# Kernel tuning notes

Measured on AMD Instinct MI355X. Metric: run time of the kernel, lower is better.

The kernel has to match this reference:

```python
import jax, jax.numpy as jnp
import numpy as np

B, S, F, H = 16, 2048, 1024, 16
D = F // H
EPS = 1e-5


def setup_inputs() -> dict:
    key = jax.random.key(0)
    ks = jax.random.split(key, 10)
    scale = 1.0 / np.sqrt(F)
    return {
        "x": jax.random.normal(ks[0], (B, S, F), jnp.float32),
        "Wq": jax.random.normal(ks[1], (F, F), jnp.float32) * scale,
        "bq": jnp.zeros((F,), jnp.float32),
        "Wk": jax.random.normal(ks[2], (F, F), jnp.float32) * scale,
        "bk": jnp.zeros((F,), jnp.float32),
        "Wv": jax.random.normal(ks[3], (F, F), jnp.float32) * scale,
        "bv": jnp.zeros((F,), jnp.float32),
        "Wo": jax.random.normal(ks[4], (F, F), jnp.float32) * scale,
        "bo": jnp.zeros((F,), jnp.float32),
        "gamma": jnp.ones((F,), jnp.float32),
        "beta": jnp.zeros((F,), jnp.float32),
    }


def reference(x, Wq, bq, Wk, bk, Wv, bv, Wo, bo, gamma, beta):
    # x: (B, S, F). Dropout is identity in eval mode.
    b, s, f = x.shape
    q = (x @ Wq + bq).reshape(b, s, H, D)
    k = (x @ Wk + bk).reshape(b, s, H, D)
    v = (x @ Wv + bv).reshape(b, s, H, D)
    # Faithful to source: the einsum (applied to permuted tensors) contracts
    # across HEADS at each sequence position -> scores (B, S, H, H).
    energy = jnp.einsum('bshd,bsgd->bshg', q, k) / (D ** 0.5)
    attn = jax.nn.softmax(energy, axis=-1)  # softmax over key-head axis
    out = jnp.einsum('bshg,bsgd->bshd', attn, v).reshape(b, s, f)
    out = out @ Wo + bo
    # LayerNorm over last dim (eps=1e-5, affine)
    mu = jnp.mean(out, axis=-1, keepdims=True)
    var = jnp.mean((out - mu) ** 2, axis=-1, keepdims=True)
    return (out - mu) * jax.lax.rsqrt(var + EPS) * gamma + beta
```

## Files before the change

### kernel.cpp

```cpp
#include <hip/hip_runtime.h>
#include <hip/hip_bf16.h>
#include <stdint.h>

#define MM   32768
#define FFD  1024
#define NQKV 3072

typedef __bf16 bf16x8 __attribute__((ext_vector_type(8)));
typedef float  f32x4  __attribute__((ext_vector_type(4)));

__device__ __forceinline__ unsigned short f2bf_bits(float f){
  __hip_bfloat16 h = __float2bfloat16(f);
  unsigned short u;
  __builtin_memcpy(&u, &h, 2);
  return u;
}

__device__ __forceinline__ void gld16(const void* g, void* l){
  const unsigned int* gu = (const unsigned int*)g;
  unsigned int* lu = (unsigned int*)l;
  __builtin_amdgcn_global_load_lds(
      (const __attribute__((address_space(1))) unsigned int*)gu,
      (__attribute__((address_space(3))) unsigned int*)lu,
      16, 0, 0);
}

__global__ __launch_bounds__(256) void k_convert_bf16(const float* __restrict__ in,
                                                      unsigned short* __restrict__ out,
                                                      int n4){
  int i = blockIdx.x * 256 + threadIdx.x;
  if (i >= n4) return;
  float4 v = ((const float4*)in)[i];
  ushort4 r;
  r.x = f2bf_bits(v.x); r.y = f2bf_bits(v.y);
  r.z = f2bf_bits(v.z); r.w = f2bf_bits(v.w);
  ((ushort4*)out)[i] = r;
}

__global__ __launch_bounds__(256) void k_transpose_bf16(const float* __restrict__ in,
                                                        unsigned short* __restrict__ out,
                                                        int rows, int cols){
  __shared__ float tile[32][33];
  int bc = blockIdx.x * 32, br = blockIdx.y * 32;
  int tx = threadIdx.x, ty = threadIdx.y;
  #pragma unroll
  for (int j = 0; j < 32; j += 8)
    tile[ty + j][tx] = in[(size_t)(br + ty + j) * cols + bc + tx];
  __syncthreads();
  #pragma unroll
  for (int j = 0; j < 32; j += 8)
    out[(size_t)(bc + ty + j) * rows + br + tx] = f2bf_bits(tile[tx][ty + j]);
}

template <bool BF16OUT>
__global__ __launch_bounds__(256) void k_gemm_bt(
    const unsigned short* __restrict__ A,
    const unsigned short* __restrict__ Bt,
    const float* __restrict__ b0, const float* __restrict__ b1, const float* __restrict__ b2,
    void* __restrict__ Cout, int M, int N, int K)
{
  __shared__ unsigned short As[128 * 64];
  __shared__ unsigned short Bs[128 * 64];

  const int tid  = threadIdx.x;
  const int lane = tid & 63;
  const int wave = tid >> 6;
  const int wr = wave >> 1, wc = wave & 1;
  const int quad = lane >> 4, lrow = lane & 15;

  const long rowBase = (long)blockIdx.y * 128;
  const long colBase = (long)blockIdx.x * 128;

  f32x4 acc[4][4];
  #pragma unroll
  for (int i = 0; i < 4; i++)
    #pragma unroll
    for (int j = 0; j < 4; j++)
      acc[i][j] = (f32x4){0.f, 0.f, 0.f, 0.f};

  const unsigned short* ga = A  + (rowBase + (tid >> 2)) * (long)K + (tid & 3) * 8;
  const unsigned short* gb = Bt + (colBase + (tid >> 2)) * (long)K + (tid & 3) * 8;
  unsigned short* la = As + tid * 8;
  unsigned short* lb = Bs + tid * 8;
  const long rstep = 64L * K;

  const int nk = K >> 6;
  for (int kt = 0; kt < nk; kt++){
    __syncthreads();
    gld16(ga,               la);
    gld16(ga + rstep,       la + 2048);
    gld16(ga + 32,          la + 4096);
    gld16(ga + 32 + rstep,  la + 6144);
    gld16(gb,               lb);
    gld16(gb + rstep,       lb + 2048);
    gld16(gb + 32,          lb + 4096);
    gld16(gb + 32 + rstep,  lb + 6144);
    __syncthreads();

    #pragma unroll
    for (int kk = 0; kk < 2; kk++){
      const unsigned short* Ah = As + kk * 4096;
      const unsigned short* Bh = Bs + kk * 4096;
      bf16x8 af[4], bfr[4];
      #pragma unroll
      for (int i = 0; i < 4; i++)
        af[i]  = *(const bf16x8*)(Ah + (wr * 64 + i * 16 + lrow) * 32 + quad * 8);
      #pragma unroll
      for (int j = 0; j < 4; j++)
        bfr[j] = *(const bf16x8*)(Bh + (wc * 64 + j * 16 + lrow) * 32 + quad * 8);

      #pragma unroll
      for (int i = 0; i < 4; i++)
        #pragma unroll
        for (int j = 0; j < 4; j++)
          acc[i][j] = __builtin_amdgcn_mfma_f32_16x16x32_bf16(af[i], bfr[j], acc[i][j], 0, 0, 0);
    }

    ga += 64; gb += 64;
  }

  #pragma unroll
  for (int j = 0; j < 4; j++){
    long col = colBase + wc * 64 + j * 16 + lrow;
    const float* bp = (col < 1024) ? b0 : ((col < 2048) ? b1 : b2);
    float bias = bp[col & 1023];
    #pragma unroll
    for (int i = 0; i < 4; i++){
      long row0 = rowBase + wr * 64 + i * 16 + quad * 4;
      #pragma unroll
      for (int r = 0; r < 4; r++){
        float v = acc[i][j][r] + bias;
        if constexpr (BF16OUT)
          ((unsigned short*)Cout)[(row0 + r) * (long)N + col] = f2bf_bits(v);
        else
          ((float*)Cout)[(row0 + r) * (long)N + col] = v;
      }
    }
  }
}

__global__ __launch_bounds__(256) void k_attention(const unsigned short* __restrict__ qkv,
                                                   unsigned short* __restrict__ aout){
  constexpr int QOFF = 0;
  constexpr int KOFF = 1152;
  constexpr int VOFF = 2304;
  constexpr int POFF = 4864;
  constexpr int PER  = 5504;
  __shared__ unsigned short smem[4 * PER];

  const int lane = threadIdx.x & 63;
  const int wave = threadIdx.x >> 6;
  const int pos  = blockIdx.x * 4 + wave;
  const int quad = lane >> 4, lidx = lane & 15;

  unsigned short* base = smem + wave * PER;
  unsigned short* Qb = base + QOFF;
  unsigned short* Kb = base + KOFF;
  unsigned short* Vt = base + VOFF;
  unsigned short* Pb = base + POFF;

  {
    uint4 z = {0u, 0u, 0u, 0u};
    *(uint4*)(Vt + lane * 40 + 16) = z;
    *(uint4*)(Vt + lane * 40 + 24) = z;
    *(uint2*)(Pb + (lane >> 2) * 40 + 16 + (lane & 3) * 4) = make_uint2(0u, 0u);
  }

  const unsigned short* src = qkv + (size_t)pos * 3072;
  #pragma unroll
  for (int i = 0; i < 6; i++){
    int c = i * 64 + lane;
    uint4 u = *(const uint4*)(src + c * 8);
    if (i < 4){
      unsigned short* mb = (c < 128) ? Qb : Kb;
      int cc = c & 127;
      *(uint4*)(mb + (cc >> 3) * 72 + (cc & 7) * 8) = u;
    } else {
      int cv = c - 256;
      int g = cv >> 3, d0 = (cv & 7) * 8;
      const unsigned short* us = (const unsigned short*)&u;
      #pragma unroll
      for (int t = 0; t < 8; t++) Vt[(d0 + t) * 40 + g] = us[t];
    }
  }
  __syncthreads();

  f32x4 s = (f32x4){0.f, 0.f, 0.f, 0.f};
  #pragma unroll
  for (int kk = 0; kk < 2; kk++){
    bf16x8 a = *(const bf16x8*)(Qb + lidx * 72 + kk * 32 + quad * 8);
    bf16x8 b = *(const bf16x8*)(Kb + lidx * 72 + kk * 32 + quad * 8);
    s = __builtin_amdgcn_mfma_f32_16x16x32_bf16(a, b, s, 0, 0, 0);
  }

  #pragma unroll
  for (int r = 0; r < 4; r++){
    float v = s[r] * 0.125f;
    float m = v;
    m = fmaxf(m, __shfl_xor(m, 1));
    m = fmaxf(m, __shfl_xor(m, 2));
    m = fmaxf(m, __shfl_xor(m, 4));
    m = fmaxf(m, __shfl_xor(m, 8));
    float e = __expf(v - m);
    float sum = e;
    sum += __shfl_xor(sum, 1);
    sum += __shfl_xor(sum, 2);
    sum += __shfl_xor(sum, 4);
    sum += __shfl_xor(sum, 8);
    float p = e / sum;
    Pb[(quad * 4 + r) * 40 + lidx] = f2bf_bits(p);
  }
  __syncthreads();

  f32x4 o[4];
  #pragma unroll
  for (int n4 = 0; n4 < 4; n4++){
    bf16x8 a = *(const bf16x8*)(Pb + lidx * 40 + quad * 8);
    bf16x8 b = *(const bf16x8*)(Vt + (n4 * 16 + lidx) * 40 + quad * 8);
    o[n4] = __builtin_amdgcn_mfma_f32_16x16x32_bf16(a, b, (f32x4){0.f,0.f,0.f,0.f}, 0, 0, 0);
  }

  #pragma unroll
  for (int n4 = 0; n4 < 4; n4++)
    #pragma unroll
    for (int r = 0; r < 4; r++)
      Qb[(quad * 4 + r) * 72 + n4 * 16 + lidx] = f2bf_bits(o[n4][r]);
  __syncthreads();

  unsigned short* dst = aout + (size_t)pos * 1024;
  #pragma unroll
  for (int t = 0; t < 2; t++){
    int j = lane * 2 + t;
    int h = j >> 3, dc = j & 7;
    uint4 u = *(const uint4*)(Qb + h * 72 + dc * 8);
    *(uint4*)(dst + j * 8) = u;
  }
}

__global__ __launch_bounds__(256) void k_ln(float* __restrict__ out,
                                            const float* __restrict__ gamma,
                                            const float* __restrict__ beta){
  __shared__ float red[8];
  int tid = threadIdx.x;
  float4* rowp = (float4*)(out + (size_t)blockIdx.x * 1024);
  float4 v = rowp[tid];
  float s  = v.x + v.y + v.z + v.w;
  float ss = v.x * v.x + v.y * v.y + v.z * v.z + v.w * v.w;
  #pragma unroll
  for (int off = 32; off > 0; off >>= 1){
    s  += __shfl_down(s, off);
    ss += __shfl_down(ss, off);
  }
  if ((tid & 63) == 0){ red[tid >> 6] = s; red[4 + (tid >> 6)] = ss; }
  __syncthreads();
  float S  = red[0] + red[1] + red[2] + red[3];
  float SS = red[4] + red[5] + red[6] + red[7];
  float mean = S * (1.0f / 1024.0f);
  float var  = SS * (1.0f / 1024.0f) - mean * mean;
  float rstd = rsqrtf(var + 1e-5f);
  float4 g = ((const float4*)gamma)[tid];
  float4 b = ((const float4*)beta)[tid];
  v.x = (v.x - mean) * rstd * g.x + b.x;
  v.y = (v.y - mean) * rstd * g.y + b.y;
  v.z = (v.z - mean) * rstd * g.z + b.z;
  v.w = (v.w - mean) * rstd * g.w + b.w;
  rowp[tid] = v;
}

extern "C" void kernel_launch(void* const* d_in, const int* in_sizes, int n_in,
                              void* d_out, int out_size, void* d_ws, size_t ws_size,
                              hipStream_t stream){
  const float* x     = (const float*)d_in[0];
  const float* Wq    = (const float*)d_in[1];
  const float* bq    = (const float*)d_in[2];
  const float* Wk    = (const float*)d_in[3];
  const float* bk    = (const float*)d_in[4];
  const float* Wv    = (const float*)d_in[5];
  const float* bv    = (const float*)d_in[6];
  const float* Wo    = (const float*)d_in[7];
  const float* bo    = (const float*)d_in[8];
  const float* gamma = (const float*)d_in[9];
  const float* beta  = (const float*)d_in[10];
  float* out = (float*)d_out;

  char* ws = (char*)d_ws;
  unsigned short* Wqkv_t = (unsigned short*)ws;
  unsigned short* Wo_t   = (unsigned short*)(ws + 6291456);
  unsigned short* xb     = (unsigned short*)(ws + 8388608);
  unsigned short* qkv    = (unsigned short*)(ws + 75497472);
  unsigned short* aout   = xb;

  k_convert_bf16<<<32768, 256, 0, stream>>>(x, xb, (MM * FFD) / 4);

  dim3 tb(32, 8), tg(32, 32);
  k_transpose_bf16<<<tg, tb, 0, stream>>>(Wq, Wqkv_t,                1024, 1024);
  k_transpose_bf16<<<tg, tb, 0, stream>>>(Wk, Wqkv_t + 1024 * 1024,  1024, 1024);
  k_transpose_bf16<<<tg, tb, 0, stream>>>(Wv, Wqkv_t + 2048 * 1024,  1024, 1024);
  k_transpose_bf16<<<tg, tb, 0, stream>>>(Wo, Wo_t,                  1024, 1024);

  k_gemm_bt<true><<<dim3(NQKV / 128, MM / 128), 256, 0, stream>>>(
      xb, Wqkv_t, bq, bk, bv, qkv, MM, NQKV, FFD);

  k_attention<<<MM / 4, 256, 0, stream>>>(qkv, aout);

  k_gemm_bt<false><<<dim3(FFD / 128, MM / 128), 256, 0, stream>>>(
      aout, Wo_t, bo, bo, bo, out, MM, FFD, FFD);

  k_ln<<<MM, 256, 0, stream>>>(out, gamma, beta);
}
```

Baseline: 706.0 us.

## Rewrite GEMM with 256x256 tiles, 4-stage LDS pipeline, swizzle and XCD remap

Rewrites the bf16 GEMM kernel to use 512-thread blocks computing 256x256 output tiles. Global-to-LDS loads go through a 4-deep ring buffer (128KB LDS) with explicit vmcnt waits and raw barriers, so loads overlap MFMA work. It also adds XOR swizzling of LDS rows to avoid bank conflicts, a block-id remap across 8 XCDs for L2 locality, and raised wave priority around MFMA bursts. The cost is heavy LDS use and more register pressure, which limits occupancy, plus fragile manual waitcnt logic.

```diff
diff --git a/kernel.cpp b/kernel.cpp
--- a/kernel.cpp
+++ b/kernel.cpp
@@ -24,6 +24,10 @@
       (__attribute__((address_space(3))) unsigned int*)lu,
       16, 0, 0);
 }
+
+#define BARRIER() do { asm volatile("" ::: "memory"); \
+                       __builtin_amdgcn_s_barrier();  \
+                       asm volatile("" ::: "memory"); } while(0)
 
 __global__ __launch_bounds__(256) void k_convert_bf16(const float* __restrict__ in,
                                                       unsigned short* __restrict__ out,
@@ -53,83 +57,116 @@
 }
 
 template <bool BF16OUT>
-__global__ __launch_bounds__(256) void k_gemm_bt(
+__global__ __launch_bounds__(512, 2) void k_gemm_bt(
     const unsigned short* __restrict__ A,
     const unsigned short* __restrict__ Bt,
     const float* __restrict__ b0, const float* __restrict__ b1, const float* __restrict__ b2,
     void* __restrict__ Cout, int M, int N, int K)
 {
-  __shared__ unsigned short As[128 * 64];
-  __shared__ unsigned short Bs[128 * 64];
+  __shared__ alignas(16) char smem[131072];
 
   const int tid  = threadIdx.x;
   const int lane = tid & 63;
   const int wave = tid >> 6;
-  const int wr = wave >> 1, wc = wave & 1;
+  const int wr = wave >> 2, wc = wave & 3;
   const int quad = lane >> 4, lrow = lane & 15;
-
-  const long rowBase = (long)blockIdx.y * 128;
-  const long colBase = (long)blockIdx.x * 128;
-
-  f32x4 acc[4][4];
-  #pragma unroll
-  for (int i = 0; i < 4; i++)
+  const int sa = ((lrow >> 1) & 3) << 4;
+
+  const int nwgx = gridDim.x;
+  int nwg = nwgx * gridDim.y;
+  int bid = blockIdx.y * nwgx + blockIdx.x;
+  int cpx = nwg >> 3;
+  int nid = (bid & 7) * cpx + (bid >> 3);
+  int by = nid / nwgx;
+  int bx = nid - by * nwgx;
+
+  const long rowBase = (long)by * 256;
+  const long colBase = (long)bx * 256;
+
+  f32x4 acc[8][4];
+  #pragma unroll
+  for (int i = 0; i < 8; i++)
     #pragma unroll
     for (int j = 0; j < 4; j++)
       acc[i][j] = (f32x4){0.f, 0.f, 0.f, 0.f};
 
-  const unsigned short* ga = A  + (rowBase + (tid >> 2)) * (long)K + (tid & 3) * 8;
-  const unsigned short* gb = Bt + (colBase + (tid >> 2)) * (long)K + (tid & 3) * 8;
-  unsigned short* la = As + tid * 8;
-  unsigned short* lb = Bs + tid * 8;
-  const long rstep = 64L * K;
-
-  const int nk = K >> 6;
-  for (int kt = 0; kt < nk; kt++){
-    __syncthreads();
-    gld16(ga,               la);
-    gld16(ga + rstep,       la + 2048);
-    gld16(ga + 32,          la + 4096);
-    gld16(ga + 32 + rstep,  la + 6144);
-    gld16(gb,               lb);
-    gld16(gb + rstep,       lb + 2048);
-    gld16(gb + 32,          lb + 4096);
-    gld16(gb + 32 + rstep,  lb + 6144);
-    __syncthreads();
-
+  const int swz8 = 8 * ((tid & 3) ^ ((tid >> 3) & 3));
+  const unsigned short* gA = A  + (rowBase + (tid >> 2)) * (long)K + swz8;
+  const unsigned short* gB = Bt + (colBase + (tid >> 2)) * (long)K + swz8;
+  const long hstep = 128L * K;
+
+  const int nk = K >> 5;
+
+  #pragma unroll
+  for (int tt = 0; tt < 3; ++tt){
+    char* nb = smem + tt * 32768;
+    gld16(gA + tt * 32,         nb +         tid * 16);
+    gld16(gA + tt * 32 + hstep, nb +  8192 + tid * 16);
+    gld16(gB + tt * 32,         nb + 16384 + tid * 16);
+    gld16(gB + tt * 32 + hstep, nb + 24576 + tid * 16);
+  }
+  asm volatile("s_waitcnt vmcnt(8)" ::: "memory");
+  BARRIER();
+
+  for (int t = 0; t < nk; ++t){
+    char* buf = smem + (t & 3) * 32768;
+    char* nb  = smem + ((t + 3) & 3) * 32768;
+    const unsigned short* sA = gA + (long)(t + 3) * 32;
+    const unsigned short* sB = gB + (long)(t + 3) * 32;
+    const bool st = (t < nk - 3);
+
+    bf16x8 bfr[4];
     #pragma unroll
-    for (int kk = 0; kk < 2; kk++){
-      const unsigned short* Ah = As + kk * 4096;
-      const unsigned short* Bh = Bs + kk * 4096;
-      bf16x8 af[4], bfr[4];
+    for (int p = 0; p < 2; ++p){
+      bf16x8 af[4];
+      const char* ab = buf + wr * 8192 + p * 4096 + lrow * 64 + ((quad * 16) ^ sa);
       #pragma unroll
-      for (int i = 0; i < 4; i++)
-        af[i]  = *(const bf16x8*)(Ah + (wr * 64 + i * 16 + lrow) * 32 + quad * 8);
+      for (int f = 0; f < 4; ++f)
+        af[f] = *(const bf16x8*)(ab + f * 1024);
+      if (p == 0){
+        const char* bb = buf + 16384 + wc * 4096 + lrow * 64 + ((quad * 16) ^ sa);
+        #pragma unroll
+        for (int n = 0; n < 4; ++n)
+          bfr[n] = *(const bf16x8*)(bb + n * 1024);
+        if (st){
+          gld16(sA,         nb +        tid * 16);
+          gld16(sA + hstep, nb + 8192 + tid * 16);
+        }
+      } else {
+        if (st){
+          gld16(sB,         nb + 16384 + tid * 16);
+          gld16(sB + hstep, nb + 24576 + tid * 16);
+        }
+      }
+      BARRIER();
+      __builtin_amdgcn_s_setprio(1);
       #pragma unroll
-      for (int j = 0; j < 4; j++)
-        bfr[j] = *(const bf16x8*)(Bh + (wc * 64 + j * 16 + lrow) * 32 + quad * 8);
-
-      #pragma unroll
-      for (int i = 0; i < 4; i++)
+      for (int f = 0; f < 4; ++f)
         #pragma unroll
-        for (int j = 0; j < 4; j++)
-          acc[i][j] = __builtin_amdgcn_mfma_f32_16x16x32_bf16(af[i], bfr[j], acc[i][j], 0, 0, 0);
+        for (int n = 0; n < 4; ++n)
+          acc[p * 4 + f][n] =
+              __builtin_amdgcn_mfma_f32_16x16x32_bf16(af[f], bfr[n], acc[p * 4 + f][n], 0, 0, 0);
+      __builtin_amdgcn_s_setprio(0);
+      if (p == 1){
+        if (st)               asm volatile("s_waitcnt vmcnt(8)" ::: "memory");
+        else if (t == nk - 3) asm volatile("s_waitcnt vmcnt(4)" ::: "memory");
+        else if (t == nk - 2) asm volatile("s_waitcnt vmcnt(0)" ::: "memory");
+      }
+      BARRIER();
     }
-
-    ga += 64; gb += 64;
-  }
-
-  #pragma unroll
-  for (int j = 0; j < 4; j++){
-    long col = colBase + wc * 64 + j * 16 + lrow;
+  }
+
+  #pragma unroll
+  for (int n = 0; n < 4; ++n){
+    long col = colBase + wc * 64 + n * 16 + lrow;
     const float* bp = (col < 1024) ? b0 : ((col < 2048) ? b1 : b2);
     float bias = bp[col & 1023];
     #pragma unroll
-    for (int i = 0; i < 4; i++){
-      long row0 = rowBase + wr * 64 + i * 16 + quad * 4;
+    for (int m = 0; m < 8; ++m){
+      long row0 = rowBase + wr * 128 + (m >> 2) * 64 + (m & 3) * 16 + quad * 4;
       #pragma unroll
-      for (int r = 0; r < 4; r++){
-        float v = acc[i][j][r] + bias;
+      for (int r = 0; r < 4; ++r){
+        float v = acc[m][n][r] + bias;
         if constexpr (BF16OUT)
           ((unsigned short*)Cout)[(row0 + r) * (long)N + col] = f2bf_bits(v);
         else
@@ -298,12 +335,12 @@
   k_transpose_bf16<<<tg, tb, 0, stream>>>(Wv, Wqkv_t + 2048 * 1024,  1024, 1024);
   k_transpose_bf16<<<tg, tb, 0, stream>>>(Wo, Wo_t,                  1024, 1024);
 
-  k_gemm_bt<true><<<dim3(NQKV / 128, MM / 128), 256, 0, stream>>>(
+  k_gemm_bt<true><<<dim3(NQKV / 256, MM / 256), 512, 0, stream>>>(
       xb, Wqkv_t, bq, bk, bv, qkv, MM, NQKV, FFD);
 
   k_attention<<<MM / 4, 256, 0, stream>>>(qkv, aout);
 
-  k_gemm_bt<false><<<dim3(FFD / 128, MM / 128), 256, 0, stream>>>(
+  k_gemm_bt<false><<<dim3(FFD / 256, MM / 256), 512, 0, stream>>>(
       aout, Wo_t, bo, bo, bo, out, MM, FFD, FFD);
 
   k_ln<<<MM, 256, 0, stream>>>(out, gamma, beta);
```

Result: faster. 655.3 us (-7.2%).
